# Performance work log

Hardware: AMD Instinct MI355X
Metric: run time of the kernel (lower is better)

The kernel has to match this reference:

```python
import jax, jax.numpy as jnp
import numpy as np

WAY = 5
TEMPERATURE = 0.2
TEMPERATURE_ATTN = 5.0
BN_EPS = 1e-5


def bn_apply(x, p):
    # p: (4, C) = gamma, beta, running_mean, running_var (eval-mode BatchNorm)
    g, b, m, v = p[0], p[1], p[2], p[3]
    sh = (1, -1) + (1,) * (x.ndim - 2)
    return (x - m.reshape(sh)) * (g.reshape(sh) / jnp.sqrt(v.reshape(sh) + BN_EPS)) + b.reshape(sh)


def conv3d(x, w, pad):
    return jax.lax.conv_general_dilated(
        x, w, (1, 1, 1), [(pad[0], pad[0]), (pad[1], pad[1]), (pad[2], pad[2])],
        dimension_numbers=('NCDHW', 'OIDHW', 'NCDHW'))


def sepconv4d(x, conv2_w, bn2, conv1_w, bn1, proj_w, bnp):
    # x: (b, c, u, v, h, w). conv2: (k,k,1) kernel over (u,v); conv1: (1,k,k) over (h,w).
    b, c, u, v, h, w = x.shape
    y = x.reshape(b, c, u, v, h * w)
    y = bn_apply(conv3d(y, conv2_w, (1, 1, 0)), bn2)
    y = jax.nn.relu(y)
    y = y.reshape(b, c, u * v, h, w)
    y = bn_apply(conv3d(y, conv1_w, (0, 1, 1)), bn1)
    # 1x1 projection (pointwise over channels) + BN
    y = jnp.einsum('oc,bcxhw->boxhw', proj_w, y)
    y = bn_apply(y, bnp)
    return y.reshape(b, -1, u, v, h, w)


def cca(x, c1, c2):
    def branch(z):
        z = sepconv4d(z, *c1)
        z = jax.nn.relu(z)
        z = sepconv4d(z, *c2)
        return z
    perm = (0, 1, 4, 5, 2, 3)
    return branch(x) + jnp.transpose(branch(jnp.transpose(x, perm)), perm)


def gaussian_normalize(x, axis, eps=1e-5):
    m = jnp.mean(x, axis=axis, keepdims=True)
    v = jnp.var(x, axis=axis, keepdims=True, ddof=1)  # torch.var is unbiased
    return (x - m) / jnp.sqrt(v + eps)


def setup_inputs() -> dict:
    key = jax.random.key(0)
    ks = jax.random.split(key, 16)

    def bn_params(k, c):
        k1, k2, k3, k4 = jax.random.split(k, 4)
        g = 1.0 + 0.1 * jax.random.normal(k1, (c,), jnp.float32)
        b = 0.1 * jax.random.normal(k2, (c,), jnp.float32)
        m = 0.1 * jax.random.normal(k3, (c,), jnp.float32)
        v = 1.0 + 0.1 * jax.random.uniform(k4, (c,), jnp.float32)
        return jnp.stack([g, b, m, v])

    return {
        'spt': jax.random.normal(ks[0], (1, 5, 640, 10, 10), jnp.float32),
        'qry': jax.random.normal(ks[1], (75, 640, 10, 10), jnp.float32),
        'w_1x1': jax.random.normal(ks[2], (64, 640), jnp.float32) * 0.04,
        'bn_1x1': bn_params(ks[3], 64),
        'c1_conv2_w': jax.random.normal(ks[4], (1, 1, 3, 3, 1), jnp.float32) * 0.33,
        'c1_bn2': bn_params(ks[5], 1),
        'c1_conv1_w': jax.random.normal(ks[6], (1, 1, 1, 3, 3), jnp.float32) * 0.33,
        'c1_bn1': bn_params(ks[7], 1),
        'c1_proj_w': jax.random.normal(ks[8], (16, 1), jnp.float32),
        'c1_bnp': bn_params(ks[9], 16),
        'c2_conv2_w': jax.random.normal(ks[10], (16, 16, 3, 3, 1), jnp.float32) * 0.083,
        'c2_bn2': bn_params(ks[11], 16),
        'c2_conv1_w': jax.random.normal(ks[12], (16, 16, 1, 3, 3), jnp.float32) * 0.083,
        'c2_bn1': bn_params(ks[13], 16),
        'c2_proj_w': jax.random.normal(ks[14], (1, 16), jnp.float32) * 0.25,
        'c2_bnp': bn_params(ks[15], 1),
    }


def reference(spt, qry, w_1x1, bn_1x1,
              c1_conv2_w, c1_bn2, c1_conv1_w, c1_bn1, c1_proj_w, c1_bnp,
              c2_conv2_w, c2_bn2, c2_conv1_w, c2_bn1, c2_proj_w, c2_bnp):
    s = spt[0]                                   # (way, C, H, W)
    s = s - s.mean(axis=1, keepdims=True)        # normalize_feature
    q = qry - qry.mean(axis=1, keepdims=True)

    def cca1x1(x):
        y = jnp.einsum('oc,bchw->bohw', w_1x1, x)
        return jax.nn.relu(bn_apply(y, bn_1x1))

    sf = cca1x1(s)
    qf = cca1x1(q)
    sf = sf / jnp.maximum(jnp.linalg.norm(sf, axis=1, keepdims=True), 1e-8)
    qf = qf / jnp.maximum(jnp.linalg.norm(qf, axis=1, keepdims=True), 1e-8)

    # 4D correlation (avoids the repeat-induced 6D blowup of the original)
    corr = jnp.einsum('ncij,qckl->qnijkl', sf, qf)  # (Q, way, Hs, Ws, Hq, Wq)
    Q, way, Hs, Ws, Hq, Wq = corr.shape

    c1 = (c1_conv2_w, c1_bn2, c1_conv1_w, c1_bn1, c1_proj_w, c1_bnp)
    c2 = (c2_conv2_w, c2_bn2, c2_conv1_w, c2_bn1, c2_proj_w, c2_bnp)
    corr = cca(corr.reshape(Q * way, 1, Hs, Ws, Hq, Wq), c1, c2)

    corr_s = corr.reshape(Q, way, Hs * Ws, Hq, Wq)
    corr_q = corr.reshape(Q, way, Hs, Ws, Hq * Wq)
    corr_s = gaussian_normalize(corr_s, axis=2)
    corr_q = gaussian_normalize(corr_q, axis=4)
    corr_s = jax.nn.softmax(corr_s / TEMPERATURE_ATTN, axis=2).reshape(Q, way, Hs, Ws, Hq, Wq)
    corr_q = jax.nn.softmax(corr_q / TEMPERATURE_ATTN, axis=4).reshape(Q, way, Hs, Ws, Hq, Wq)

    attn_s = corr_s.sum(axis=(4, 5))             # (Q, way, Hs, Ws)
    attn_q = corr_q.sum(axis=(2, 3))             # (Q, way, Hq, Wq)

    spt_att = (attn_s[:, :, None] * s[None]).mean(axis=(-1, -2))       # (Q, way, C)
    qry_att = (attn_q[:, :, None] * q[:, None]).mean(axis=(-1, -2))    # (Q, way, C)
    qry_pooled = q.mean(axis=(-1, -2))                                  # (Q, C)

    num = jnp.sum(spt_att * qry_att, axis=-1)
    den = (jnp.maximum(jnp.linalg.norm(spt_att, axis=-1), 1e-8) *
           jnp.maximum(jnp.linalg.norm(qry_att, axis=-1), 1e-8))
    sim = (num / den) / TEMPERATURE
    return sim, qry_pooled
```

## Files before the change

### kernel.cpp

```cpp
#include <hip/hip_runtime.h>


#define NITEM 375

#define OFF_XTS 0
#define OFF_XTQ 160000
#define OFF_MP  2560000
#define OFF_SF  2568000
#define OFF_QF  2600000
#define OFF_RA  3080000
#define OFF_RB  6830000
#define OFF_PRM 10655000

#define PK2F 232
#define PK1F 1512
#define WSUMF 2792
#define SCVF 2856
#define SHVF 2920
#define PKWF 2984

#define Y1S   20480
#define Y1HALF 16000
#define ZPB   116480
#define Y2S   116512
#define Y2HALF 16128
#define LDS_TOTAL 148768

typedef float f4v __attribute__((ext_vector_type(4)));
typedef float f32x4 __attribute__((ext_vector_type(4)));
typedef _Float16 half8v __attribute__((ext_vector_type(8)));
typedef __fp16 fp16x2 __attribute__((ext_vector_type(2)));
typedef unsigned int u32x4 __attribute__((ext_vector_type(4)));
typedef unsigned int u32x2 __attribute__((ext_vector_type(2)));

__device__ __forceinline__ unsigned int pkrtz(float a, float b) {
  union { fp16x2 h; unsigned int u; } cv;
  cv.h = __builtin_amdgcn_cvt_pkrtz(a, b);
  return cv.u;
}

__global__ __launch_bounds__(256) void k_prep(
    const float* __restrict__ w1x1,  const float* __restrict__ bn1x1,
    const float* __restrict__ c1c2w, const float* __restrict__ c1bn2,
    const float* __restrict__ c1c1w, const float* __restrict__ c1bn1,
    const float* __restrict__ c1pj,  const float* __restrict__ c1bnp,
    const float* __restrict__ c2c2w, const float* __restrict__ c2bn2,
    const float* __restrict__ c2c1w, const float* __restrict__ c2bn1,
    const float* __restrict__ c2pj,  const float* __restrict__ c2bnp,
    float* __restrict__ prm)
{
  const int t = threadIdx.x;
  const float eps = 1e-5f;

  for (int idx = t; idx < 144; idx += 256) {
    int ds = idx / 16, i = idx % 16;
    float spv = c2bnp[0] / sqrtf(c2bnp[3] + eps);
    float acc = 0.f;
    for (int o = 0; o < 16; ++o) {
      float s1 = c2bn1[o] / sqrtf(c2bn1[48 + o] + eps);
      acc += c2pj[o] * s1 * c2c1w[(o * 16 + i) * 9 + ds];
    }
    prm[idx] = spv * acc;
  }
  for (int i = t; i < 16; i += 256) {
    float s = c1bnp[i] / sqrtf(c1bnp[48 + i] + eps);
    prm[144 + i] = s * c1pj[i];
    prm[160 + i] = c1bnp[16 + i] - c1bnp[32 + i] * s;
  }
  for (int o = t; o < 16; o += 256) {
    float s = c2bn2[o] / sqrtf(c2bn2[48 + o] + eps);
    prm[176 + o] = s;
    prm[192 + o] = c2bn2[16 + o] - c2bn2[32 + o] * s;
  }
  for (int k = t; k < 9; k += 256) {
    prm[208 + k] = c1c2w[k];
    prm[217 + k] = c1c1w[k];
  }
  if (t == 0) {
    float S2 = c1bn2[0] / sqrtf(c1bn2[3] + eps);
    prm[226] = S2;
    prm[227] = c1bn2[1] - c1bn2[2] * S2;
    float S1 = c1bn1[0] / sqrtf(c1bn1[3] + eps);
    prm[228] = S1;
    prm[229] = c1bn1[1] - c1bn1[2] * S1;
    float spv = c2bnp[0] / sqrtf(c2bnp[3] + eps);
    float k0 = 0.f;
    for (int o = 0; o < 16; ++o) {
      float s1 = c2bn1[o] / sqrtf(c2bn1[48 + o] + eps);
      k0 += c2pj[o] * (c2bn1[16 + o] - c2bn1[32 + o] * s1);
    }
    prm[230] = spv * (k0 - c2bnp[2]) + c2bnp[1];
    prm[231] = 0.f;
  }
  for (int o = t; o < 64; o += 256) {
    float s = 0.f;
    for (int c = 0; c < 640; ++c) s += w1x1[o * 640 + c];
    prm[WSUMF + o] = s;
    float scv = bn1x1[o] / sqrtf(bn1x1[192 + o] + eps);
    prm[SCVF + o] = scv;
    prm[SHVF + o] = bn1x1[64 + o] - bn1x1[128 + o] * scv;
  }
  __syncthreads();

  _Float16* pk2 = (_Float16*)(prm + PK2F);
  for (int idx = t; idx < 2560; idx += 256) {
    int c = idx >> 9, rem = idx & 511;
    int ln = rem >> 3, j = rem & 7;
    int o = ln & 15, qq = ln >> 4;
    int tap = 2 * c + (qq >> 1);
    int i = (qq & 1) * 8 + j;
    float v = (tap < 9) ? c2c2w[(o * 16 + i) * 9 + tap] : 0.f;
    pk2[idx] = (_Float16)v;
  }
  _Float16* pk1 = (_Float16*)(prm + PK1F);
  for (int idx = t; idx < 2560; idx += 256) {
    int c = idx >> 9, rem = idx & 511;
    int ln = rem >> 3, j = rem & 7;
    int m = ln & 15, qq = ln >> 4;
    int k = c * 32 + qq * 8 + j;
    int tp = k >> 4, i = k & 15;
    float v = (m == 0 && tp < 9) ? prm[tp * 16 + i] : 0.f;
    pk1[idx] = (_Float16)v;
  }
}

__global__ __launch_bounds__(256) void k_prepw(
    const float* __restrict__ w1x1, float* __restrict__ prm)
{
  _Float16* pkw = (_Float16*)(prm + PKWF);
  const int base = blockIdx.x * 800;
  for (int r = threadIdx.x; r < 800; r += 256) {
    int idx = base + r;
    int fi = idx >> 9, rem = idx & 511;
    int ln = rem >> 3, j = rem & 7;
    int cc = fi / 10, r2 = fi - cc * 10;
    int mt = r2 >> 1, kk = r2 & 1;
    int m = mt * 16 + (ln & 15);
    int k = cc * 64 + kk * 32 + ((ln >> 4) & 3) * 8 + j;
    float v = (m < 64) ? w1x1[m * 640 + k] : (m == 64 ? 1.f : 0.f);
    pkw[idx] = (_Float16)v;
  }
}

__global__ __launch_bounds__(512) void k_feat(
    const float* __restrict__ spt, const float* __restrict__ qry,
    float* __restrict__ ws, float* __restrict__ out)
{
  __shared__ __align__(16) _Float16 XTL[112 * 72];
  __shared__ __align__(16) float OUT[64 * 104];
  __shared__ __align__(16) float mrow[112];
  __shared__ __align__(16) float rn[112];
  __shared__ float CS[512];
  __shared__ float RS[640];
  __shared__ float msumL;

  const int b = blockIdx.x, t = threadIdx.x;
  const int lane = t & 63, wvv = t >> 6;
  const int n0 = lane & 15, qd = (lane >> 4) & 3;
  const float* src = (b < 5) ? spt + b * 64000 : qry + (b - 5) * 64000;
  float* dst = (b < 5) ? ws + OFF_SF + b * 6400 : ws + OFF_QF + (b - 5) * 6400;
  unsigned int* xtg = (unsigned int*)(ws + ((b < 5) ? (OFF_XTS + b * 32000)
                                                    : (OFF_XTQ + (b - 5) * 32000)));
  const float* prm = ws + OFF_PRM;
  const _Float16* pkw = (const _Float16*)(prm + PKWF);

  for (int idx = t; idx < 12 * 36; idx += 512)
    ((unsigned int*)(XTL + 100 * 72))[idx] = 0u;

  const int chp = t >> 3, part = t & 7;
  const int pLo = part * 13, pHi = (pLo + 13 < 100) ? pLo + 13 : 100;

  f32x4 acc[5];
  #pragma unroll
  for (int ti = 0; ti < 5; ++ti) { acc[ti][0]=0.f; acc[ti][1]=0.f; acc[ti][2]=0.f; acc[ti][3]=0.f; }

  for (int cc = 0; cc < 10; ++cc) {
    __syncthreads();
    for (int u = t; u < 800; u += 512) {
      int cp = u / 25, p4 = u - cp * 25;
      const float* r0 = src + (cc * 64 + 2 * cp) * 100 + p4 * 4;
      f4v a = *(const f4v*)r0;
      f4v c1 = *(const f4v*)(r0 + 100);
      #pragma unroll
      for (int e = 0; e < 4; ++e)
        *(unsigned int*)(XTL + (p4 * 4 + e) * 72 + 2 * cp) = pkrtz(a[e], c1[e]);
    }
    __syncthreads();
    for (int u = t; u < 3200; u += 512) {
      int p = u >> 5, cp = u & 31;
      xtg[p * 320 + cc * 32 + cp] = *(const unsigned int*)(XTL + p * 72 + 2 * cp);
    }
    #pragma unroll
    for (int kk = 0; kk < 2; ++kk) {
      #pragma unroll
      for (int ti = 0; ti < 5; ++ti) {
        int idx = wvv + ti * 8; if (idx > 34) idx = 34;
        int mt = idx / 7, nt = idx - mt * 7;
        half8v av = *(const half8v*)(pkw + (cc * 10 + mt * 2 + kk) * 512 + lane * 8);
        half8v bv = *(const half8v*)(XTL + (nt * 16 + n0) * 72 + kk * 32 + qd * 8);
        acc[ti] = __builtin_amdgcn_mfma_f32_16x16x32_f16(av, bv, acc[ti], 0, 0, 0);
      }
    }
    {
      float s = 0.f;
      for (int p = pLo; p < pHi; ++p) s += (float)XTL[p * 72 + chp];
      CS[t] = s;
    }
    __syncthreads();
    if (t < 64) {
      float s = 0.f;
      #pragma unroll
      for (int k = 0; k < 8; ++k) s += CS[t * 8 + k];
      RS[cc * 64 + t] = s;
    }
  }
  #pragma unroll
  for (int ti = 0; ti < 5; ++ti) {
    int idx = wvv + ti * 8; if (idx > 34) idx = 34;
    int mt = idx / 7, nt = idx - mt * 7;
    if (mt == 4 && qd == 0) {
      int p = nt * 16 + n0;
      mrow[p] = acc[ti][0] * (1.f / 640.f);
    }
  }
  __syncthreads();
  if (t == 0) { float s = 0.f; for (int p = 0; p < 100; ++p) s += mrow[p]; msumL = s; }
  #pragma unroll
  for (int ti = 0; ti < 5; ++ti) {
    int idx = wvv + ti * 8; if (idx > 34) idx = 34;
    int mt = idx / 7, nt = idx - mt * 7;
    if (mt < 4) {
      int p = nt * 16 + n0;
      if (p < 100) {
        float mp = mrow[p];
        #pragma unroll
        for (int r = 0; r < 4; ++r) {
          int o = mt * 16 + qd * 4 + r;
          float v = acc[ti][r] - prm[WSUMF + o] * mp;
          v = prm[SCVF + o] * v + prm[SHVF + o];
          OUT[o * 104 + p] = v > 0.f ? v : 0.f;
        }
      }
    }
  }
  __syncthreads();
  if (t < 100) {
    float s = 0.f;
    for (int o = 0; o < 64; ++o) { float v = OUT[o * 104 + t]; s += v * v; }
    float nr = sqrtf(s);
    rn[t] = 1.f / (nr > 1e-8f ? nr : 1e-8f);
    ws[OFF_MP + b * 100 + t] = mrow[t];
  }
  __syncthreads();
  for (int idx = t; idx < 1600; idx += 512) {
    int o = idx / 25, pq = idx - o * 25;
    f4v v = *(const f4v*)(OUT + o * 104 + pq * 4);
    f4v r4 = *(const f4v*)(rn + pq * 4);
    #pragma unroll
    for (int e = 0; e < 4; ++e) v[e] *= r4[e];
    *(f4v*)(dst + o * 100 + pq * 4) = v;
  }
  if (b >= 5) {
    const float msum = msumL;
    for (int gc = t; gc < 640; gc += 512)
      out[375 + (b - 5) * 640 + gc] = (RS[gc] - msum) * 0.01f;
  }
}

__global__ __launch_bounds__(1024) __attribute__((amdgpu_waves_per_eu(4, 4)))
void k_cca(float* __restrict__ ws)
{
  extern __shared__ char smem[];
  _Float16* T2h = (_Float16*)smem;
  float* sfL  = (float*)(smem + 20480);
  float* qfL  = (float*)(smem + 46080);
  float* CORR = (float*)(smem + 71680);
  float* T1   = (float*)(smem + 20480);

  const float* prm = ws + OFF_PRM;
  const int bid = blockIdx.x;
  const int it = bid >> 1, br = bid & 1;
  const int q = it / 5, n = it % 5;
  const int t = threadIdx.x;
  const int lane = t & 63, wv = t >> 6;
  const int n0 = lane & 15, qd = (lane >> 4) & 3;
  const int qh = qd >> 1, ih = qd & 1;

  const _Float16* pk2 = (const _Float16*)(prm + PK2F);
  const _Float16* pk1 = (const _Float16*)(prm + PK1F);
  half8v A2[5], A1[5];
  #pragma unroll
  for (int c = 0; c < 5; ++c) {
    A2[c] = *(const half8v*)(pk2 + c * 512 + lane * 8);
    A1[c] = *(const half8v*)(pk1 + c * 512 + lane * 8);
  }
  float sc2[4], bc2[4];
  #pragma unroll
  for (int r = 0; r < 4; ++r) { sc2[r] = prm[176 + qd * 4 + r]; bc2[r] = prm[192 + qd * 4 + r]; }

  const int d1E[5] = {-1,-1, 0, 0, 1}, d2E[5] = {-1, 1, 0,-1, 1};
  const int d1O[5] = {-1, 0, 0, 1, 0}, d2O[5] = { 0,-1, 1, 0, 0};

  int D1[5];
  #pragma unroll
  for (int c = 0; c < 5; ++c)
    D1[c] = (qh ? (d1O[c] * 10 + d2O[c]) : (d1E[c] * 10 + d2E[c])) * 16;
  const int BY = Y2S + ih * Y2HALF;
  const int ihY1 = ih * Y1HALF;

  {
    const f4v* sf4 = (const f4v*)(ws + OFF_SF + n * 6400);
    const f4v* qf4 = (const f4v*)(ws + OFF_QF + q * 6400);
    f4v* sL4 = (f4v*)sfL; f4v* qL4 = (f4v*)qfL;
    for (int idx = t; idx < 1600; idx += 1024) { sL4[idx] = sf4[idx]; qL4[idx] = qf4[idx]; }
  }
  __syncthreads();

  if (t < 625) {
    const int ij0 = (t / 25) * 4, kl0 = (t % 25) * 4;
    f4v acc4[4];
    #pragma unroll
    for (int jj = 0; jj < 4; ++jj) { acc4[jj][0]=0.f; acc4[jj][1]=0.f; acc4[jj][2]=0.f; acc4[jj][3]=0.f; }
    for (int c = 0; c < 64; ++c) {
      f4v sv = *(const f4v*)(sfL + c * 100 + ij0);
      f4v qv = *(const f4v*)(qfL + c * 100 + kl0);
      #pragma unroll
      for (int jj = 0; jj < 4; ++jj)
        #pragma unroll
        for (int e = 0; e < 4; ++e) acc4[jj][e] += sv[jj] * qv[e];
    }
    if (br == 0) {
      #pragma unroll
      for (int jj = 0; jj < 4; ++jj) *(f4v*)(CORR + (ij0 + jj) * 100 + kl0) = acc4[jj];
    } else {
      #pragma unroll
      for (int kk = 0; kk < 4; ++kk) {
        f4v tr;
        #pragma unroll
        for (int jj = 0; jj < 4; ++jj) tr[jj] = acc4[jj][kk];
        *(f4v*)(CORR + (kl0 + kk) * 100 + ij0) = tr;
      }
    }
  }
  __syncthreads();

  const float S2 = prm[226], B2 = prm[227], S1 = prm[228], B1 = prm[229];

  for (int idx = t; idx < 2500; idx += 1024) {
    int f = idx / 25, sq = (idx % 25) * 4;
    int f1 = f / 10, f2 = f - f1 * 10;
    f4v acc; acc[0]=0.f; acc[1]=0.f; acc[2]=0.f; acc[3]=0.f;
    #pragma unroll
    for (int du = 0; du < 3; ++du) {
      int nf1 = f1 + du - 1;
      if ((unsigned)nf1 >= 10u) continue;
      #pragma unroll
      for (int dv = 0; dv < 3; ++dv) {
        int nf2 = f2 + dv - 1;
        if ((unsigned)nf2 >= 10u) continue;
        float w = prm[208 + du * 3 + dv];
        f4v xv = *(const f4v*)(CORR + (nf1 * 10 + nf2) * 100 + sq);
        #pragma unroll
        for (int e = 0; e < 4; ++e) acc[e] += w * xv[e];
      }
    }
    #pragma unroll
    for (int e = 0; e < 4; ++e) { float v = S2 * acc[e] + B2; acc[e] = v > 0.f ? v : 0.f; }
    *(f4v*)(T1 + f * 100 + sq) = acc;
  }
  __syncthreads();

  if (t < 1000) {
    const int f = t / 10, s1 = t - (t / 10) * 10;
    const float* rowB = T1 + f * 100;
    f4v r[3][3];
    float w[3][3];
    #pragma unroll
    for (int dh = 0; dh < 3; ++dh) {
      int rr = s1 + dh - 1;
      bool okr = (unsigned)rr < 10u;
      int rc = rr < 0 ? 0 : (rr > 9 ? 9 : rr);
      const float* rp = rowB + rc * 10;
      r[dh][0] = *(const f4v*)(rp);
      r[dh][1] = *(const f4v*)(rp + 4);
      r[dh][2] = *(const f4v*)(rp + 8);
      #pragma unroll
      for (int dw = 0; dw < 3; ++dw) w[dh][dw] = okr ? prm[217 + dh * 3 + dw] : 0.f;
    }
    float o[10];
    #pragma unroll
    for (int s2 = 0; s2 < 10; ++s2) {
      float a = 0.f;
      #pragma unroll
      for (int dh = 0; dh < 3; ++dh)
        #pragma unroll
        for (int dw = 0; dw < 3; ++dw) {
          int col = s2 + dw - 1;
          if (col < 0 || col > 9) continue;
          a += w[dh][dw] * r[dh][col >> 2][col & 3];
        }
      o[s2] = a;
    }
    unsigned int* dst = (unsigned int*)((char*)T2h + (f * 100 + s1 * 10) * 2);
    #pragma unroll
    for (int k = 0; k < 5; ++k)
      dst[k] = pkrtz(S1 * o[2 * k] + B1, S1 * o[2 * k + 1] + B1);
  }
  __syncthreads();

  #define GEN_Y1(F1N)                                                          \
    if (t < 1000) {                                                            \
      const int _sl = (F1N) % 3;                                               \
      const float t2 = (float)T2h[(F1N) * 1000 + t];                           \
      unsigned int d[8];                                                       \
      _Pragma("unroll")                                                        \
      for (int j = 0; j < 8; ++j) {                                            \
        float ya = fmaxf(prm[144 + 2 * j] * t2 + prm[160 + 2 * j], 0.f);       \
        float yb = fmaxf(prm[145 + 2 * j] * t2 + prm[161 + 2 * j], 0.f);       \
        d[j] = pkrtz(ya, yb);                                                  \
      }                                                                        \
      u32x4 lo, hi;                                                            \
      lo[0]=d[0]; lo[1]=d[1]; lo[2]=d[2]; lo[3]=d[3];                          \
      hi[0]=d[4]; hi[1]=d[5]; hi[2]=d[6]; hi[3]=d[7];                          \
      *(u32x4*)(smem + Y1S + _sl * 32000 + t * 16) = lo;                       \
      *(u32x4*)(smem + Y1S + _sl * 32000 + Y1HALF + t * 16) = hi;              \
    }

  GEN_Y1(0)
  GEN_Y1(1)
  if (t >= 1000 && t < 1004) *(unsigned int*)(smem + ZPB + (t - 1000) * 4) = 0u;
  __syncthreads();

  const float Cf = prm[230];
  float* resb = ws + (br ? OFF_RB : OFF_RA) + it * 10000;

  for (int g = 0; g < 10; ++g) {
    const int sl0 = g % 3, slP = (g + 1) % 3, slM = (g + 2) % 3;
    const int baseM = Y1S + slM * 32000;
    const int base0 = Y1S + sl0 * 32000;
    const int baseP = Y1S + slP * 32000;
    const bool okM = (g >= 1), okP = (g <= 8);
    int Bc[5]; bool v1c[5];
    #pragma unroll
    for (int c = 0; c < 5; ++c) {
      int bE = (d1E[c] < 0 ? baseM : (d1E[c] > 0 ? baseP : base0)) + d2E[c] * 1600;
      int bO = (d1O[c] < 0 ? baseM : (d1O[c] > 0 ? baseP : base0)) + d2O[c] * 1600;
      Bc[c] = (qh ? bO : bE) + ihY1;
      bool vE = d1E[c] < 0 ? okM : (d1E[c] > 0 ? okP : true);
      bool vO = (c == 4) ? false : (d1O[c] < 0 ? okM : (d1O[c] > 0 ? okP : true));
      v1c[c] = qh ? vO : vE;
    }

    for (int tile = wv; tile < 63; tile += 16) {
      const int p = tile * 16 + n0;
      const int pcp = p < 1000 ? p : 999;
      const int pp = pcp * 16;
      const int f2 = pcp / 100;
      const bool fm = f2 > 0, fp = f2 < 9;
      f32x4 acc; acc[0]=0.f; acc[1]=0.f; acc[2]=0.f; acc[3]=0.f;
      #pragma unroll
      for (int c = 0; c < 5; ++c) {
        bool v2E = d2E[c] < 0 ? fm : (d2E[c] > 0 ? fp : true);
        bool v2O = d2O[c] < 0 ? fm : (d2O[c] > 0 ? fp : true);
        bool v = v1c[c] && (qh ? v2O : v2E);
        int addr = v ? (Bc[c] + pp) : ZPB;
        half8v b = *(const half8v*)(smem + addr);
        acc = __builtin_amdgcn_mfma_f32_16x16x32_f16(A2[c], b, acc, 0, 0, 0);
      }
      float v0 = fmaxf(sc2[0] * acc[0] + bc2[0], 0.f);
      float v1 = fmaxf(sc2[1] * acc[1] + bc2[1], 0.f);
      float v2 = fmaxf(sc2[2] * acc[2] + bc2[2], 0.f);
      float v3 = fmaxf(sc2[3] * acc[3] + bc2[3], 0.f);
      u32x2 wq; wq[0] = pkrtz(v0, v1); wq[1] = pkrtz(v2, v3);
      *(u32x2*)(smem + Y2S + qh * Y2HALF + p * 16 + ih * 8) = wq;
    }
    __syncthreads();

    for (int tile = wv; tile < 63; tile += 16) {
      const int p = tile * 16 + n0;
      const int pcp = p < 1000 ? p : 999;
      const int b0 = BY + pcp * 16;
      const int f2 = pcp / 100;
      const int s = pcp - f2 * 100;
      const int s1 = s / 10, s2 = s - s1 * 10;
      const bool rm = s1 > 0, rp = s1 < 9, cm = s2 > 0, cp = s2 < 9;
      f32x4 acc; acc[0]=0.f; acc[1]=0.f; acc[2]=0.f; acc[3]=0.f;
      #pragma unroll
      for (int c = 0; c < 5; ++c) {
        bool vE = (d1E[c] < 0 ? rm : (d1E[c] > 0 ? rp : true)) &&
                  (d2E[c] < 0 ? cm : (d2E[c] > 0 ? cp : true));
        bool vO = (c == 4) ? false :
                  ((d1O[c] < 0 ? rm : (d1O[c] > 0 ? rp : true)) &&
                   (d2O[c] < 0 ? cm : (d2O[c] > 0 ? cp : true)));
        bool v = qh ? vO : vE;
        int addr = v ? (b0 + D1[c]) : ZPB;
        half8v b = *(const half8v*)(smem + addr);
        acc = __builtin_amdgcn_mfma_f32_16x16x32_f16(A1[c], b, acc, 0, 0, 0);
      }
      if (qd == 0 && p < 1000) {
        const int fg = g * 10 + f2;
        const int pos = br ? (s * 100 + fg) : (fg * 100 + s);
        resb[pos] = acc[0] + Cf;
      }
    }
    if (g + 2 <= 9) { GEN_Y1(g + 2) }
    __syncthreads();
  }
  #undef GEN_Y1
}

__global__ __launch_bounds__(256) void k_post(float* __restrict__ ws,
                                              float* __restrict__ out)
{
  __shared__ float F[10000];
  __shared__ float mc[100], ic[100], rc[100];
  __shared__ float mr[100], ir[100], rr[100];
  __shared__ float asL[100], aqL[100], msL[100], mqL[100];
  __shared__ float alph[2];
  __shared__ float red[12];
  const int it = blockIdx.x, t = threadIdx.x;
  const int q = it / 5, n = it % 5;

  const f4v* ra4 = (const f4v*)(ws + OFF_RA + it * 10000);
  const f4v* rb4 = (const f4v*)(ws + OFF_RB + it * 10000);
  f4v* F4 = (f4v*)F;
  for (int idx = t; idx < 2500; idx += 256) {
    f4v a = ra4[idx], b = rb4[idx];
    #pragma unroll
    for (int e = 0; e < 4; ++e) a[e] += b[e];
    F4[idx] = a;
  }
  if (t < 100) msL[t] = ws[OFF_MP + n * 100 + t];
  else if (t < 200) mqL[t - 100] = ws[OFF_MP + (5 + q) * 100 + t - 100];
  __syncthreads();

  if (t < 100) {
    float s = 0.f;
    for (int ij = 0; ij < 100; ++ij) s += F[ij * 100 + t];
    float m = s * 0.01f;
    float ss = 0.f;
    for (int ij = 0; ij < 100; ++ij) { float d = F[ij * 100 + t] - m; ss += d * d; }
    float inv = 1.f / (sqrtf(ss * (1.f / 99.f) + 1e-5f) * 5.f);
    float den = 0.f;
    for (int ij = 0; ij < 100; ++ij) den += __expf((F[ij * 100 + t] - m) * inv);
    mc[t] = m; ic[t] = inv; rc[t] = 1.f / den;
  } else if (t < 200) {
    const int r = t - 100;
    float s = 0.f;
    for (int kl = 0; kl < 100; ++kl) s += F[r * 100 + kl];
    float m = s * 0.01f;
    float ss = 0.f;
    for (int kl = 0; kl < 100; ++kl) { float d = F[r * 100 + kl] - m; ss += d * d; }
    float inv = 1.f / (sqrtf(ss * (1.f / 99.f) + 1e-5f) * 5.f);
    float den = 0.f;
    for (int kl = 0; kl < 100; ++kl) den += __expf((F[r * 100 + kl] - m) * inv);
    mr[r] = m; ir[r] = inv; rr[r] = 1.f / den;
  }
  __syncthreads();
  if (t < 100) {
    float s = 0.f;
    for (int kl = 0; kl < 100; ++kl)
      s += __expf((F[t * 100 + kl] - mc[kl]) * ic[kl]) * rc[kl];
    asL[t] = s;
  } else if (t < 200) {
    const int r = t - 100;
    float s2 = 0.f;
    for (int ij = 0; ij < 100; ++ij)
      s2 += __expf((F[ij * 100 + r] - mr[ij]) * ir[ij]) * rr[ij];
    aqL[r] = s2;
  }
  __syncthreads();
  if (t < 2) {
    float s = 0.f;
    for (int p = 0; p < 100; ++p) s += t ? (aqL[p] * mqL[p]) : (asL[p] * msL[p]);
    alph[t] = s;
  }
  __syncthreads();

  const unsigned int* xs = (const unsigned int*)(ws + OFF_XTS + n * 32000);
  const unsigned int* xq = (const unsigned int*)(ws + OFF_XTQ + q * 32000);
  const float als = alph[0], alq = alph[1];
  float dot = 0.f, na = 0.f, nb = 0.f;
  for (int u = t; u < 320; u += 256) {
    float s0 = 0.f, s1 = 0.f, q0 = 0.f, q1 = 0.f;
    for (int p = 0; p < 100; ++p) {
      union { unsigned int u; fp16x2 h; } a, bq;
      a.u = xs[p * 320 + u];
      bq.u = xq[p * 320 + u];
      float ap = asL[p], qp = aqL[p];
      s0 += ap * (float)a.h[0]; s1 += ap * (float)a.h[1];
      q0 += qp * (float)bq.h[0]; q1 += qp * (float)bq.h[1];
    }
    float sa0 = (s0 - als) * 0.01f, sa1 = (s1 - als) * 0.01f;
    float qa0 = (q0 - alq) * 0.01f, qa1 = (q1 - alq) * 0.01f;
    dot += sa0 * qa0 + sa1 * qa1;
    na  += sa0 * sa0 + sa1 * sa1;
    nb  += qa0 * qa0 + qa1 * qa1;
  }
  #pragma unroll
  for (int off = 32; off > 0; off >>= 1) {
    dot += __shfl_down(dot, off);
    na  += __shfl_down(na, off);
    nb  += __shfl_down(nb, off);
  }
  const int wid = t >> 6, lanei = t & 63;
  if (lanei == 0) { red[wid * 3 + 0] = dot; red[wid * 3 + 1] = na; red[wid * 3 + 2] = nb; }
  __syncthreads();
  if (t == 0) {
    dot = red[0] + red[3] + red[6] + red[9];
    na  = red[1] + red[4] + red[7] + red[10];
    nb  = red[2] + red[5] + red[8] + red[11];
    float ns = sqrtf(na); ns = ns > 1e-8f ? ns : 1e-8f;
    float nq2 = sqrtf(nb); nq2 = nq2 > 1e-8f ? nq2 : 1e-8f;
    out[it] = dot / (ns * nq2) * 5.f;
  }
}

extern "C" void kernel_launch(void* const* d_in, const int* in_sizes, int n_in,
                              void* d_out, int out_size, void* d_ws, size_t ws_size,
                              hipStream_t stream)
{
  (void)in_sizes; (void)n_in; (void)out_size; (void)ws_size;
  const float* spt    = (const float*)d_in[0];
  const float* qry    = (const float*)d_in[1];
  const float* w1x1   = (const float*)d_in[2];
  const float* bn1x1  = (const float*)d_in[3];
  const float* c1c2w  = (const float*)d_in[4];
  const float* c1bn2  = (const float*)d_in[5];
  const float* c1c1w  = (const float*)d_in[6];
  const float* c1bn1  = (const float*)d_in[7];
  const float* c1pj   = (const float*)d_in[8];
  const float* c1bnp  = (const float*)d_in[9];
  const float* c2c2w  = (const float*)d_in[10];
  const float* c2bn2  = (const float*)d_in[11];
  const float* c2c1w  = (const float*)d_in[12];
  const float* c2bn1  = (const float*)d_in[13];
  const float* c2pj   = (const float*)d_in[14];
  const float* c2bnp  = (const float*)d_in[15];
  float* ws  = (float*)d_ws;
  float* out = (float*)d_out;

  k_prep<<<1, 256, 0, stream>>>(w1x1, bn1x1,
                                c1c2w, c1bn2, c1c1w, c1bn1, c1pj, c1bnp,
                                c2c2w, c2bn2, c2c1w, c2bn1, c2pj, c2bnp,
                                ws + OFF_PRM);
  k_prepw<<<64, 256, 0, stream>>>(w1x1, ws + OFF_PRM);
  k_feat<<<80, 512, 0, stream>>>(spt, qry, ws, out);

  (void)hipFuncSetAttribute((const void*)k_cca,
                            hipFuncAttributeMaxDynamicSharedMemorySize, LDS_TOTAL);
  k_cca<<<NITEM * 2, 1024, LDS_TOTAL, stream>>>(ws);

  k_post<<<NITEM, 256, 0, stream>>>(ws, out);
}
```

Baseline: 357.2 us.

## Pad Y1 slabs with zero halos and precompute per-tile addresses

The Y1 ring buffer is re-laid out with zero-filled guard regions before each half and an extra zeroed slab at the boundaries, so the first conv's loads no longer need per-element validity checks or a fallback to the zero pad address. The per-tile addresses, validity flags and output positions for the second conv are computed once before the g loop and kept in registers, and the tile loops are fully unrolled. This removes integer index arithmetic and branching from the inner MFMA loops. In exchange it uses more LDS (about 160 KB instead of 149 KB), holds around 20 extra address registers per thread, and adds zero-fill stores at setup and at g==8.

```diff
diff --git a/kernel.cpp b/kernel.cpp
--- a/kernel.cpp
+++ b/kernel.cpp
@@ -19,12 +19,15 @@
 #define SHVF 2920
 #define PKWF 2984
 
-#define Y1S   20480
-#define Y1HALF 16000
-#define ZPB   116480
-#define Y2S   116512
-#define Y2HALF 16128
-#define LDS_TOTAL 148768
+#define Y1S2     20480
+#define Y1GAP    1600
+#define Y1HSTR   17600
+#define Y1SSTR   35200
+#define Y1BASE   (Y1S2 + Y1GAP)
+#define ZPB2     127680
+#define Y2S2     127712
+#define Y2HALF2  16128
+#define LDS_TOTAL2 159968
 
 typedef float f4v __attribute__((ext_vector_type(4)));
 typedef float f32x4 __attribute__((ext_vector_type(4)));
@@ -301,12 +304,36 @@
   const int d1E[5] = {-1,-1, 0, 0, 1}, d2E[5] = {-1, 1, 0,-1, 1};
   const int d1O[5] = {-1, 0, 0, 1, 0}, d2O[5] = { 0,-1, 1, 0, 0};
 
-  int D1[5];
+  int pp1[4], st1[4], addr2[4][5], posB[4];
+  bool pv[4];
   #pragma unroll
-  for (int c = 0; c < 5; ++c)
-    D1[c] = (qh ? (d1O[c] * 10 + d2O[c]) : (d1E[c] * 10 + d2E[c])) * 16;
-  const int BY = Y2S + ih * Y2HALF;
-  const int ihY1 = ih * Y1HALF;
+  for (int ti = 0; ti < 4; ++ti) {
+    int tile = wv + ti * 16; if (tile > 62) tile = 62;
+    const int p = tile * 16 + n0;
+    const int pcp = p < 1000 ? p : 999;
+    pp1[ti] = pcp * 16;
+    st1[ti] = Y2S2 + qh * Y2HALF2 + p * 16 + ih * 8;
+    pv[ti] = (qd == 0) && (p < 1000);
+    const int f2 = pcp / 100;
+    const int s = pcp - f2 * 100;
+    const int s1 = s / 10, s2 = s - s1 * 10;
+    const bool rm = s1 > 0, rp = s1 < 9, cm = s2 > 0, cp2 = s2 < 9;
+    const int b0 = Y2S2 + ih * Y2HALF2 + pcp * 16;
+    #pragma unroll
+    for (int c = 0; c < 5; ++c) {
+      const bool vE = (d1E[c] < 0 ? rm : (d1E[c] > 0 ? rp : true)) &&
+                      (d2E[c] < 0 ? cm : (d2E[c] > 0 ? cp2 : true));
+      const bool vO = (c == 4) ? false :
+                      ((d1O[c] < 0 ? rm : (d1O[c] > 0 ? rp : true)) &&
+                       (d2O[c] < 0 ? cm : (d2O[c] > 0 ? cp2 : true)));
+      const bool v = qh ? vO : vE;
+      const int D1c = (qh ? (d1O[c] * 10 + d2O[c]) : (d1E[c] * 10 + d2E[c])) * 16;
+      addr2[ti][c] = v ? (b0 + D1c) : ZPB2;
+    }
+    posB[ti] = br ? (s * 100 + f2) : (f2 * 100 + s);
+  }
+  const int posStride = br ? 10 : 1000;
+  const int ihbase = Y1BASE + ih * Y1HSTR;
 
   {
     const f4v* sf4 = (const f4v*)(ws + OFF_SF + n * 6400);
@@ -422,88 +449,79 @@
       u32x4 lo, hi;                                                            \
       lo[0]=d[0]; lo[1]=d[1]; lo[2]=d[2]; lo[3]=d[3];                          \
       hi[0]=d[4]; hi[1]=d[5]; hi[2]=d[6]; hi[3]=d[7];                          \
-      *(u32x4*)(smem + Y1S + _sl * 32000 + t * 16) = lo;                       \
-      *(u32x4*)(smem + Y1S + _sl * 32000 + Y1HALF + t * 16) = hi;              \
+      *(u32x4*)(smem + Y1BASE + _sl * Y1SSTR + t * 16) = lo;                   \
+      *(u32x4*)(smem + Y1BASE + _sl * Y1SSTR + Y1HSTR + t * 16) = hi;          \
     }
 
   GEN_Y1(0)
   GEN_Y1(1)
-  if (t >= 1000 && t < 1004) *(unsigned int*)(smem + ZPB + (t - 1000) * 4) = 0u;
+  {
+    u32x4 zz; zz[0] = 0u; zz[1] = 0u; zz[2] = 0u; zz[3] = 0u;
+    for (int idx = t; idx < 700; idx += 1024) {
+      const int r = idx / 100;
+      *(u32x4*)(smem + Y1S2 + r * Y1HSTR + (idx - r * 100) * 16) = zz;
+    }
+    for (int idx = t; idx < 2000; idx += 1024) {
+      const int h = idx >= 1000 ? 1 : 0;
+      *(u32x4*)(smem + Y1BASE + 2 * Y1SSTR + h * Y1HSTR + (idx - h * 1000) * 16) = zz;
+    }
+    if (t < 2) *(u32x4*)(smem + ZPB2 + t * 16) = zz;
+  }
   __syncthreads();
 
   const float Cf = prm[230];
   float* resb = ws + (br ? OFF_RB : OFF_RA) + it * 10000;
+  int gp = 0;
 
   for (int g = 0; g < 10; ++g) {
-    const int sl0 = g % 3, slP = (g + 1) % 3, slM = (g + 2) % 3;
-    const int baseM = Y1S + slM * 32000;
-    const int base0 = Y1S + sl0 * 32000;
-    const int baseP = Y1S + slP * 32000;
-    const bool okM = (g >= 1), okP = (g <= 8);
-    int Bc[5]; bool v1c[5];
+    const int o0 = (g % 3) * Y1SSTR;
+    const int oP = ((g + 1) % 3) * Y1SSTR;
+    const int oM = ((g + 2) % 3) * Y1SSTR;
+    const int bM = ihbase + oM, b0s = ihbase + o0, bP = ihbase + oP;
+    int base1[5];
     #pragma unroll
     for (int c = 0; c < 5; ++c) {
-      int bE = (d1E[c] < 0 ? baseM : (d1E[c] > 0 ? baseP : base0)) + d2E[c] * 1600;
-      int bO = (d1O[c] < 0 ? baseM : (d1O[c] > 0 ? baseP : base0)) + d2O[c] * 1600;
-      Bc[c] = (qh ? bO : bE) + ihY1;
-      bool vE = d1E[c] < 0 ? okM : (d1E[c] > 0 ? okP : true);
-      bool vO = (c == 4) ? false : (d1O[c] < 0 ? okM : (d1O[c] > 0 ? okP : true));
-      v1c[c] = qh ? vO : vE;
-    }
-
-    for (int tile = wv; tile < 63; tile += 16) {
-      const int p = tile * 16 + n0;
-      const int pcp = p < 1000 ? p : 999;
-      const int pp = pcp * 16;
-      const int f2 = pcp / 100;
-      const bool fm = f2 > 0, fp = f2 < 9;
+      const int eb = (d1E[c] < 0 ? bM : (d1E[c] > 0 ? bP : b0s)) + d2E[c] * 1600;
+      const int ob = (d1O[c] < 0 ? bM : (d1O[c] > 0 ? bP : b0s)) + d2O[c] * 1600;
+      base1[c] = qh ? ob : eb;
+    }
+
+    #pragma unroll
+    for (int ti = 0; ti < 4; ++ti) {
       f32x4 acc; acc[0]=0.f; acc[1]=0.f; acc[2]=0.f; acc[3]=0.f;
       #pragma unroll
       for (int c = 0; c < 5; ++c) {
-        bool v2E = d2E[c] < 0 ? fm : (d2E[c] > 0 ? fp : true);
-        bool v2O = d2O[c] < 0 ? fm : (d2O[c] > 0 ? fp : true);
-        bool v = v1c[c] && (qh ? v2O : v2E);
-        int addr = v ? (Bc[c] + pp) : ZPB;
-        half8v b = *(const half8v*)(smem + addr);
+        half8v b = *(const half8v*)(smem + base1[c] + pp1[ti]);
         acc = __builtin_amdgcn_mfma_f32_16x16x32_f16(A2[c], b, acc, 0, 0, 0);
       }
-      float v0 = fmaxf(sc2[0] * acc[0] + bc2[0], 0.f);
-      float v1 = fmaxf(sc2[1] * acc[1] + bc2[1], 0.f);
-      float v2 = fmaxf(sc2[2] * acc[2] + bc2[2], 0.f);
-      float v3 = fmaxf(sc2[3] * acc[3] + bc2[3], 0.f);
+      const float v0 = fmaxf(sc2[0] * acc[0] + bc2[0], 0.f);
+      const float v1 = fmaxf(sc2[1] * acc[1] + bc2[1], 0.f);
+      const float v2 = fmaxf(sc2[2] * acc[2] + bc2[2], 0.f);
+      const float v3 = fmaxf(sc2[3] * acc[3] + bc2[3], 0.f);
       u32x2 wq; wq[0] = pkrtz(v0, v1); wq[1] = pkrtz(v2, v3);
-      *(u32x2*)(smem + Y2S + qh * Y2HALF + p * 16 + ih * 8) = wq;
+      *(u32x2*)(smem + st1[ti]) = wq;
     }
     __syncthreads();
 
-    for (int tile = wv; tile < 63; tile += 16) {
-      const int p = tile * 16 + n0;
-      const int pcp = p < 1000 ? p : 999;
-      const int b0 = BY + pcp * 16;
-      const int f2 = pcp / 100;
-      const int s = pcp - f2 * 100;
-      const int s1 = s / 10, s2 = s - s1 * 10;
-      const bool rm = s1 > 0, rp = s1 < 9, cm = s2 > 0, cp = s2 < 9;
+    #pragma unroll
+    for (int ti = 0; ti < 4; ++ti) {
       f32x4 acc; acc[0]=0.f; acc[1]=0.f; acc[2]=0.f; acc[3]=0.f;
       #pragma unroll
       for (int c = 0; c < 5; ++c) {
-        bool vE = (d1E[c] < 0 ? rm : (d1E[c] > 0 ? rp : true)) &&
-                  (d2E[c] < 0 ? cm : (d2E[c] > 0 ? cp : true));
-        bool vO = (c == 4) ? false :
-                  ((d1O[c] < 0 ? rm : (d1O[c] > 0 ? rp : true)) &&
-                   (d2O[c] < 0 ? cm : (d2O[c] > 0 ? cp : true)));
-        bool v = qh ? vO : vE;
-        int addr = v ? (b0 + D1[c]) : ZPB;
-        half8v b = *(const half8v*)(smem + addr);
+        half8v b = *(const half8v*)(smem + addr2[ti][c]);
         acc = __builtin_amdgcn_mfma_f32_16x16x32_f16(A1[c], b, acc, 0, 0, 0);
       }
-      if (qd == 0 && p < 1000) {
-        const int fg = g * 10 + f2;
-        const int pos = br ? (s * 100 + fg) : (fg * 100 + s);
-        resb[pos] = acc[0] + Cf;
+      if (pv[ti]) resb[posB[ti] + gp] = acc[0] + Cf;
+    }
+    if (g + 2 <= 9) { GEN_Y1(g + 2) }
+    else if (g == 8) {
+      u32x4 zz; zz[0] = 0u; zz[1] = 0u; zz[2] = 0u; zz[3] = 0u;
+      for (int idx = t; idx < 2000; idx += 1024) {
+        const int h = idx >= 1000 ? 1 : 0;
+        *(u32x4*)(smem + Y1BASE + Y1SSTR + h * Y1HSTR + (idx - h * 1000) * 16) = zz;
       }
     }
-    if (g + 2 <= 9) { GEN_Y1(g + 2) }
+    gp += posStride;
     __syncthreads();
   }
   #undef GEN_Y1
@@ -648,8 +666,8 @@
   k_feat<<<80, 512, 0, stream>>>(spt, qry, ws, out);
 
   (void)hipFuncSetAttribute((const void*)k_cca,
-                            hipFuncAttributeMaxDynamicSharedMemorySize, LDS_TOTAL);
-  k_cca<<<NITEM * 2, 1024, LDS_TOTAL, stream>>>(ws);
+                            hipFuncAttributeMaxDynamicSharedMemorySize, LDS_TOTAL2);
+  k_cca<<<NITEM * 2, 1024, LDS_TOTAL2, stream>>>(ws);
 
   k_post<<<NITEM, 256, 0, stream>>>(ws, out);
 }
```

New measurement: 340.2 us. 1.05x faster.
